# Kernel tuning notes

Hardware: AMD Instinct MI355X
Metric: run time of the kernel (lower is better)

## Reference

```python
import jax, jax.numpy as jnp
import numpy as np

SCALE = 1.0 / 8.0  # source divides sim_M by literal 8 (== sqrt(d_k=64))


def setup_inputs() -> dict:
    key = jax.random.key(0)
    ks = jax.random.split(key, 7)
    B, S, D = 16, 2048, 512  # D = n_head * d_k = 8 * 64
    s = 1.0 / np.sqrt(D)
    return {
        "x": jax.random.normal(ks[0], (B, S, D), dtype=jnp.float32),
        "Wq": jax.random.normal(ks[1], (D, D), dtype=jnp.float32) * s,
        "bq": jax.random.normal(ks[2], (D,), dtype=jnp.float32) * 0.01,
        "Wk": jax.random.normal(ks[3], (D, D), dtype=jnp.float32) * s,
        "bk": jax.random.normal(ks[4], (D,), dtype=jnp.float32) * 0.01,
        "Wv": jax.random.normal(ks[5], (D, D), dtype=jnp.float32) * s,
        "bv": jax.random.normal(ks[6], (D,), dtype=jnp.float32) * 0.01,
    }


def reference(x, Wq, bq, Wk, bk, Wv, bv):
    # Manual QKV projections (no head split, matching the source code)
    q = jnp.einsum("bsd,de->bse", x, Wq) + bq  # [B,S,D]
    k = jnp.einsum("bsd,de->bse", x, Wk) + bk  # [B,S,D]
    v = jnp.einsum("bsd,de->bse", x, Wv) + bv  # [B,S,D]
    # bmm -> softmax -> bmm attention
    sim = jnp.einsum("bqe,bke->bqk", q, k) * SCALE  # [B,S,S]
    attn = jax.nn.softmax(sim, axis=-1)
    out = jnp.einsum("bqk,bkd->bqd", attn, v)  # [B,S,D]
    return out
```

## Files before the change

kernel.cpp:

```cpp
#include <hip/hip_runtime.h>
#include <math.h>

typedef _Float16 f16;
typedef _Float16 f16x2 __attribute__((ext_vector_type(2)));
typedef _Float16 f16x8 __attribute__((ext_vector_type(8)));
typedef float f32x4 __attribute__((ext_vector_type(4)));

#define NB 16
#define SS 2048
#define DD 512

__device__ __forceinline__ void gl_lds16(const void* g, void* l) {
  __builtin_amdgcn_global_load_lds(
      (const __attribute__((address_space(1))) unsigned int*)g,
      (__attribute__((address_space(3))) unsigned int*)l, 16, 0, 0);
}

__device__ __forceinline__ int pk2(float a, float b) {
  f16x2 t = {(f16)a, (f16)b};
  return __builtin_bit_cast(int, t);
}

__global__ __launch_bounds__(256) void cast_kernel(const float* __restrict__ x,
                                                   f16* __restrict__ o) {
  size_t i = (size_t)blockIdx.x * 256 + threadIdx.x;
  const float4* p = (const float4*)x + i * 2;
  float4 a = p[0], b = p[1];
  f16x8 v = {(f16)a.x, (f16)a.y, (f16)a.z, (f16)a.w,
             (f16)b.x, (f16)b.y, (f16)b.z, (f16)b.w};
  *((f16x8*)o + i) = v;
}

__global__ __launch_bounds__(256) void transpose_kernel(const float* __restrict__ W,
                                                        f16* __restrict__ Wt) {
  __shared__ float t[32][33];
  int bx = blockIdx.x * 32, by = blockIdx.y * 32;
  int c = threadIdx.x & 31, r0 = threadIdx.x >> 5;
  for (int r = r0; r < 32; r += 8) t[r][c] = W[(size_t)(by + r) * DD + bx + c];
  __syncthreads();
  for (int r = r0; r < 32; r += 8) Wt[(size_t)(bx + r) * DD + by + c] = (f16)t[c][r];
}

__global__ __launch_bounds__(256) void gemm_kernel(
    const f16* __restrict__ A, long sAb, const f16* __restrict__ Bt, long sBb,
    f16* __restrict__ C, long sCb, int ldc, const float* __restrict__ bias,
    int bias_row, float scale) {
  A += (size_t)blockIdx.z * sAb;
  Bt += (size_t)blockIdx.z * sBb;
  C += (size_t)blockIdx.z * sCb;
  const int m0 = blockIdx.y * 128, n0 = blockIdx.x * 128;
  __shared__ f16 Ash[128 * 32];
  __shared__ f16 Bsh[128 * 32];
  const int tid = threadIdx.x, lane = tid & 63, wave = tid >> 6;
  const int wm = wave & 1, wn = wave >> 1;
  const int l15 = lane & 15, lq = lane >> 4;
  f32x4 acc[4][4] = {};
  const int srow = tid >> 2, part = tid & 3;
  const f16* gA = A + (size_t)(m0 + srow) * DD + part * 8;
  const f16* gB = Bt + (size_t)(n0 + srow) * DD + part * 8;
  f16* lA = &Ash[tid * 8];
  f16* lB = &Bsh[tid * 8];
  for (int kt = 0; kt < 16; ++kt) {
    gl_lds16(gA + kt * 32, lA);
    gl_lds16(gA + 64 * DD + kt * 32, lA + 2048);
    gl_lds16(gB + kt * 32, lB);
    gl_lds16(gB + 64 * DD + kt * 32, lB + 2048);
    __syncthreads();
    f16x8 af[4], bf[4];
#pragma unroll
    for (int i = 0; i < 4; ++i)
      af[i] = *(const f16x8*)&Ash[(64 * wm + 16 * i + l15) * 32 + lq * 8];
#pragma unroll
    for (int j = 0; j < 4; ++j)
      bf[j] = *(const f16x8*)&Bsh[(64 * wn + 16 * j + l15) * 32 + lq * 8];
#pragma unroll
    for (int i = 0; i < 4; ++i)
#pragma unroll
      for (int j = 0; j < 4; ++j)
        acc[i][j] = __builtin_amdgcn_mfma_f32_16x16x32_f16(af[i], bf[j], acc[i][j], 0, 0, 0);
    __syncthreads();
  }
#pragma unroll
  for (int i = 0; i < 4; ++i) {
    int rb = 64 * wm + 16 * i + lq * 4;
#pragma unroll
    for (int j = 0; j < 4; ++j) {
      int cc = n0 + 64 * wn + 16 * j + l15;
#pragma unroll
      for (int r = 0; r < 4; ++r) {
        int rr = m0 + rb + r;
        float bv = bias_row ? bias[rr] : bias[cc];
        C[(size_t)rr * ldc + cc] = (f16)((acc[i][j][r] + bv) * scale);
      }
    }
  }
}

__global__ __launch_bounds__(512, 2) void attn_kernel(
    const f16* __restrict__ Q, const f16* __restrict__ K,
    const f16* __restrict__ Vt, float* __restrict__ out) {
  const int id = blockIdx.x;
  const int b = (id & 7) + ((id >> 7) << 3);
  const int qt = (id >> 3) & 15;
  const int tid = threadIdx.x, lane = tid & 63, wave = tid >> 6;
  const int l15 = lane & 15, lq = lane >> 4;

  __shared__ __align__(16) f16 Kl[2][32][520];
  __shared__ __align__(16) f16 Vl[2][512][32];

  const f16* qp = Q + ((size_t)(b * SS + qt * 128 + wave * 16 + l15)) * DD + lq * 8;
  f16x8 qf[16];
#pragma unroll
  for (int kk = 0; kk < 16; ++kk) qf[kk] = *(const f16x8*)(qp + kk * 32);

  const f16* Kb = K + (size_t)b * SS * DD;
  const f16* Vb = Vt + (size_t)b * DD * SS;

  const int sdata = (lane & 3) ^ ((lane >> 3) & 3);
  const int vrow = lane >> 2;
  const int vs_off = (lq ^ ((l15 >> 1) & 3)) * 8;

  f16x8 onef;
#pragma unroll
  for (int j = 0; j < 8; ++j) onef[j] = (f16)1.0f;

  auto stage = [&](int sb, int kb) {
#pragma unroll
    for (int rr = 0; rr < 4; ++rr) {
      int row = wave * 4 + rr;
      gl_lds16(Kb + ((size_t)(kb + row)) * DD + lane * 8, &Kl[sb][row][lane * 8]);
    }
#pragma unroll
    for (int i = 0; i < 4; ++i) {
      int e0 = wave * 64 + i * 16;
      gl_lds16(Vb + (size_t)(e0 + vrow) * SS + kb + sdata * 8,
               (f16*)&Vl[sb][e0][0] + lane * 8);
    }
  };

  stage(0, 0);
  __syncthreads();

  f32x4 acco[32] = {};
  f32x4 accl = {};
  float m = -1e30f;

  for (int it = 0; it < 64; ++it) {
    const int buf = it & 1;
    if (it < 63) stage(buf ^ 1, (it + 1) * 32);
    f32x4 sa0 = {}, sa1 = {};
#pragma unroll
    for (int kk = 0; kk < 16; ++kk) {
      f16x8 b0 = *(const f16x8*)&Kl[buf][l15][kk * 32 + lq * 8];
      f16x8 b1 = *(const f16x8*)&Kl[buf][16 + l15][kk * 32 + lq * 8];
      sa0 = __builtin_amdgcn_mfma_f32_16x16x32_f16(b0, qf[kk], sa0, 0, 0, 0);
      sa1 = __builtin_amdgcn_mfma_f32_16x16x32_f16(b1, qf[kk], sa1, 0, 0, 0);
    }
    float lm = fmaxf(fmaxf(fmaxf(sa0[0], sa0[1]), fmaxf(sa0[2], sa0[3])),
                     fmaxf(fmaxf(sa1[0], sa1[1]), fmaxf(sa1[2], sa1[3])));
    if (__any(lm > m + 8.0f)) {
      float mx = lm;
      mx = fmaxf(mx, __shfl_xor(mx, 16));
      mx = fmaxf(mx, __shfl_xor(mx, 32));
      float mn = fmaxf(m, mx);
      float al = __expf(m - mn);
      m = mn;
      float alr[4];
#pragma unroll
      for (int r = 0; r < 4; ++r) alr[r] = __shfl(al, 4 * lq + r);
#pragma unroll
      for (int t = 0; t < 32; ++t)
#pragma unroll
        for (int r = 0; r < 4; ++r) acco[t][r] *= alr[r];
#pragma unroll
      for (int r = 0; r < 4; ++r) accl[r] *= alr[r];
    }
    int A0 = pk2(__expf(sa0[0] - m), __expf(sa0[1] - m));
    int A1 = pk2(__expf(sa0[2] - m), __expf(sa0[3] - m));
    int B0 = pk2(__expf(sa1[0] - m), __expf(sa1[1] - m));
    int B1 = pk2(__expf(sa1[2] - m), __expf(sa1[3] - m));
    const bool low = (lq < 2);
    int s0 = low ? B0 : A0, s1 = low ? B1 : A1;
    int X0 = __shfl_xor(s0, 32), X1 = __shfl_xor(s1, 32);
    int Y0 = low ? A0 : B0, Y1 = low ? A1 : B1;
    const bool sx = (lq == 0) || (lq == 3);
    int t0 = sx ? X0 : Y0, t1 = sx ? X1 : Y1;
    int Z0 = __shfl_xor(t0, 16), Z1 = __shfl_xor(t1, 16);
    union PU { int i[4]; f16x8 v; } pu;
    pu.i[0] = (lq == 0) ? Y0 : ((lq == 2) ? X0 : Z0);
    pu.i[1] = (lq == 0) ? Y1 : ((lq == 2) ? X1 : Z1);
    pu.i[2] = (lq == 1) ? X0 : ((lq == 3) ? Y0 : Z0);
    pu.i[3] = (lq == 1) ? X1 : ((lq == 3) ? Y1 : Z1);
    f16x8 pa = pu.v;
    accl = __builtin_amdgcn_mfma_f32_16x16x32_f16(pa, onef, accl, 0, 0, 0);
#pragma unroll
    for (int nn = 0; nn < 32; ++nn) {
      f16x8 vf = *(const f16x8*)&Vl[buf][nn * 16 + l15][vs_off];
      acco[nn] = __builtin_amdgcn_mfma_f32_16x16x32_f16(pa, vf, acco[nn], 0, 0, 0);
    }
    __syncthreads();
  }
  float inv[4];
#pragma unroll
  for (int r = 0; r < 4; ++r) inv[r] = 1.0f / accl[r];
  const size_t ob = ((size_t)(b * SS + qt * 128 + wave * 16 + 4 * lq)) * DD + l15;
#pragma unroll
  for (int nn = 0; nn < 32; ++nn)
#pragma unroll
    for (int r = 0; r < 4; ++r)
      out[ob + (size_t)r * DD + nn * 16] = acco[nn][r] * inv[r];
}

extern "C" void kernel_launch(void* const* d_in, const int* in_sizes, int n_in,
                              void* d_out, int out_size, void* d_ws, size_t ws_size,
                              hipStream_t stream) {
  const float* x = (const float*)d_in[0];
  const float* Wq = (const float*)d_in[1];
  const float* bq = (const float*)d_in[2];
  const float* Wk = (const float*)d_in[3];
  const float* bk = (const float*)d_in[4];
  const float* Wv = (const float*)d_in[5];
  const float* bv = (const float*)d_in[6];
  float* out = (float*)d_out;
  f16* ws = (f16*)d_ws;
  const size_t NX = (size_t)NB * SS * DD;
  f16* xh = ws;
  f16* Qh = ws + NX;
  f16* Kh = ws + 2 * NX;
  f16* Vth = ws + 3 * NX;
  f16* WqT = ws + 4 * NX;
  f16* WkT = WqT + DD * DD;
  f16* WvT = WkT + DD * DD;

  cast_kernel<<<NX / 8 / 256, 256, 0, stream>>>(x, xh);
  dim3 tg(16, 16);
  transpose_kernel<<<tg, 256, 0, stream>>>(Wq, WqT);
  transpose_kernel<<<tg, 256, 0, stream>>>(Wk, WkT);
  transpose_kernel<<<tg, 256, 0, stream>>>(Wv, WvT);
  gemm_kernel<<<dim3(4, 256, 1), 256, 0, stream>>>(xh, 0, WqT, 0, Qh, 0, DD, bq, 0, 0.125f);
  gemm_kernel<<<dim3(4, 256, 1), 256, 0, stream>>>(xh, 0, WkT, 0, Kh, 0, DD, bk, 0, 1.0f);
  gemm_kernel<<<dim3(16, 4, NB), 256, 0, stream>>>(WvT, 0, xh, (long)SS * DD, Vth,
                                                   (long)DD * SS, SS, bv, 1, 1.0f);
  attn_kernel<<<256, 512, 0, stream>>>(Qh, Kh, Vth, out);
}
```

Measured before the change: 392.7 us.

## Merge QKV projection GEMMs into one double-buffered launch and batch transposes

The three projection GEMMs become a single 3072-block kernel that picks the Q, K or V job from a swizzled block index, so work is spread across XCDs. The main loop gains a double-buffered LDS stage that prefetches the next K-tile while the current one is multiplied. The three weight transposes are also merged into one launch using blockIdx.z. This removes launch gaps and tail effects and overlaps global loads with MFMA work, at the cost of doubling LDS per block, which may lower occupancy.

```diff
diff --git a/kernel.cpp b/kernel.cpp
--- a/kernel.cpp
+++ b/kernel.cpp
@@ -31,8 +31,12 @@
   *((f16x8*)o + i) = v;
 }
 
-__global__ __launch_bounds__(256) void transpose_kernel(const float* __restrict__ W,
-                                                        f16* __restrict__ Wt) {
+__global__ __launch_bounds__(256) void transpose_kernel(
+    const float* __restrict__ W0, const float* __restrict__ W1,
+    const float* __restrict__ W2, f16* __restrict__ T0, f16* __restrict__ T1,
+    f16* __restrict__ T2) {
+  const float* W = (blockIdx.z == 0) ? W0 : (blockIdx.z == 1) ? W1 : W2;
+  f16* Wt = (blockIdx.z == 0) ? T0 : (blockIdx.z == 1) ? T1 : T2;
   __shared__ float t[32][33];
   int bx = blockIdx.x * 32, by = blockIdx.y * 32;
   int c = threadIdx.x & 31, r0 = threadIdx.x >> 5;
@@ -41,16 +45,46 @@
   for (int r = r0; r < 32; r += 8) Wt[(size_t)(bx + r) * DD + by + c] = (f16)t[c][r];
 }
 
-__global__ __launch_bounds__(256) void gemm_kernel(
-    const f16* __restrict__ A, long sAb, const f16* __restrict__ Bt, long sBb,
-    f16* __restrict__ C, long sCb, int ldc, const float* __restrict__ bias,
-    int bias_row, float scale) {
-  A += (size_t)blockIdx.z * sAb;
-  Bt += (size_t)blockIdx.z * sBb;
-  C += (size_t)blockIdx.z * sCb;
-  const int m0 = blockIdx.y * 128, n0 = blockIdx.x * 128;
-  __shared__ f16 Ash[128 * 32];
-  __shared__ f16 Bsh[128 * 32];
+__global__ __launch_bounds__(256) void gemm3_kernel(
+    const f16* __restrict__ xh, const f16* __restrict__ WqT,
+    const f16* __restrict__ WkT, const f16* __restrict__ WvT,
+    f16* __restrict__ Qh, f16* __restrict__ Kh, f16* __restrict__ Vth,
+    const float* __restrict__ bq, const float* __restrict__ bk,
+    const float* __restrict__ bv) {
+  const int wid = (blockIdx.x & 7) * 384 + (blockIdx.x >> 3);
+  const f16* A;
+  const f16* Bt;
+  f16* C;
+  const float* bias;
+  int m0, n0, ldc, bias_row;
+  float scale;
+  if (wid < 2048) {
+    const bool isK = wid >= 1024;
+    const int r = wid & 1023;
+    A = xh;
+    Bt = isK ? WkT : WqT;
+    C = isK ? Kh : Qh;
+    bias = isK ? bk : bq;
+    m0 = (r >> 2) * 128;
+    n0 = (r & 3) * 128;
+    ldc = DD;
+    bias_row = 0;
+    scale = isK ? 1.0f : 0.125f;
+  } else {
+    const int v = wid - 2048;
+    const int bz = v >> 6, xy = v & 63;
+    A = WvT;
+    Bt = xh + (size_t)bz * SS * DD;
+    C = Vth + (size_t)bz * (size_t)DD * SS;
+    bias = bv;
+    m0 = ((xy >> 4) & 3) * 128;
+    n0 = (xy & 15) * 128;
+    ldc = SS;
+    bias_row = 1;
+    scale = 1.0f;
+  }
+  __shared__ f16 Ash[2][128 * 32];
+  __shared__ f16 Bsh[2][128 * 32];
   const int tid = threadIdx.x, lane = tid & 63, wave = tid >> 6;
   const int wm = wave & 1, wn = wave >> 1;
   const int l15 = lane & 15, lq = lane >> 4;
@@ -58,21 +92,26 @@
   const int srow = tid >> 2, part = tid & 3;
   const f16* gA = A + (size_t)(m0 + srow) * DD + part * 8;
   const f16* gB = Bt + (size_t)(n0 + srow) * DD + part * 8;
-  f16* lA = &Ash[tid * 8];
-  f16* lB = &Bsh[tid * 8];
-  for (int kt = 0; kt < 16; ++kt) {
+  auto stage = [&](int sb, int kt) {
+    f16* lA = &Ash[sb][tid * 8];
+    f16* lB = &Bsh[sb][tid * 8];
     gl_lds16(gA + kt * 32, lA);
     gl_lds16(gA + 64 * DD + kt * 32, lA + 2048);
     gl_lds16(gB + kt * 32, lB);
     gl_lds16(gB + 64 * DD + kt * 32, lB + 2048);
-    __syncthreads();
+  };
+  stage(0, 0);
+  __syncthreads();
+  for (int kt = 0; kt < 16; ++kt) {
+    const int buf = kt & 1;
+    if (kt < 15) stage(buf ^ 1, kt + 1);
     f16x8 af[4], bf[4];
 #pragma unroll
     for (int i = 0; i < 4; ++i)
-      af[i] = *(const f16x8*)&Ash[(64 * wm + 16 * i + l15) * 32 + lq * 8];
+      af[i] = *(const f16x8*)&Ash[buf][(64 * wm + 16 * i + l15) * 32 + lq * 8];
 #pragma unroll
     for (int j = 0; j < 4; ++j)
-      bf[j] = *(const f16x8*)&Bsh[(64 * wn + 16 * j + l15) * 32 + lq * 8];
+      bf[j] = *(const f16x8*)&Bsh[buf][(64 * wn + 16 * j + l15) * 32 + lq * 8];
 #pragma unroll
     for (int i = 0; i < 4; ++i)
 #pragma unroll
@@ -233,13 +272,7 @@
   f16* WvT = WkT + DD * DD;
 
   cast_kernel<<<NX / 8 / 256, 256, 0, stream>>>(x, xh);
-  dim3 tg(16, 16);
-  transpose_kernel<<<tg, 256, 0, stream>>>(Wq, WqT);
-  transpose_kernel<<<tg, 256, 0, stream>>>(Wk, WkT);
-  transpose_kernel<<<tg, 256, 0, stream>>>(Wv, WvT);
-  gemm_kernel<<<dim3(4, 256, 1), 256, 0, stream>>>(xh, 0, WqT, 0, Qh, 0, DD, bq, 0, 0.125f);
-  gemm_kernel<<<dim3(4, 256, 1), 256, 0, stream>>>(xh, 0, WkT, 0, Kh, 0, DD, bk, 0, 1.0f);
-  gemm_kernel<<<dim3(16, 4, NB), 256, 0, stream>>>(WvT, 0, xh, (long)SS * DD, Vth,
-                                                   (long)DD * SS, SS, bv, 1, 1.0f);
+  transpose_kernel<<<dim3(16, 16, 3), 256, 0, stream>>>(Wq, Wk, Wv, WqT, WkT, WvT);
+  gemm3_kernel<<<3072, 256, 0, stream>>>(xh, WqT, WkT, WvT, Qh, Kh, Vth, bq, bk, bv);
   attn_kernel<<<256, 512, 0, stream>>>(Qh, Kh, Vth, out);
 }
```

New measurement: 395.3 us. No clear change (+0.7%).
